# Kernel optimization log

Hardware: AMD Instinct MI355X
Metric: run time of the kernel (lower is better)

The kernel has to match this reference:

```python
import jax, jax.numpy as jnp
import numpy as np


def _mlp(h, weights, biases, n_relu):
    # Linear(+ReLU) stack; ReLU on the first n_relu layers, final layer linear only.
    for i, (w, b) in enumerate(zip(weights, biases)):
        h = h @ w + b
        if i < n_relu:
            h = jax.nn.relu(h)
    return h


def setup_inputs() -> dict:
    key = jax.random.key(0)
    ks = jax.random.split(key, 12)
    B, M, E = 16384, 512, 1024

    def lin(k, fan_in, fan_out):
        # xavier-ish scaling so activations stay well-conditioned
        return jax.random.normal(k, (fan_in, fan_out), jnp.float32) * (1.0 / np.sqrt(fan_in))

    return {
        "x": jax.random.normal(ks[0], (B, M), jnp.float32),
        "rand_noise": jax.random.uniform(ks[1], (B, M), jnp.float32),
        "u_random": jax.random.uniform(ks[2], (B, M), jnp.float32),
        "marginals_min": jnp.zeros((M,), jnp.float32),
        "marginals_max": jnp.ones((M,), jnp.float32),
        "enc_w0": lin(ks[3], M, E), "enc_b0": jnp.full((E,), 0.01, jnp.float32),
        "enc_w1": lin(ks[4], E, E), "enc_b1": jnp.full((E,), 0.01, jnp.float32),
        "enc_w2": lin(ks[5], E, E), "enc_b2": jnp.full((E,), 0.01, jnp.float32),
        "enc_w3": lin(ks[6], E, E), "enc_b3": jnp.full((E,), 0.01, jnp.float32),
        "head_w0": lin(ks[7], E, E), "head_b0": jnp.full((E,), 0.01, jnp.float32),
        "head_w1": lin(ks[8], E, E), "head_b1": jnp.full((E,), 0.01, jnp.float32),
        "corruption_len": 307,
    }


def reference(x, rand_noise, u_random, marginals_min, marginals_max,
              enc_w0, enc_b0, enc_w1, enc_b1, enc_w2, enc_b2, enc_w3, enc_b3,
              head_w0, head_b0, head_w1, head_b1, corruption_len):
    B, M = x.shape
    # Vectorized equivalent of per-row randperm(m)[:corruption_len]:
    # top-k of iid uniform noise picks a uniform random subset of size k per row.
    _, idx = jax.lax.top_k(rand_noise, corruption_len)            # [B, k]
    mask = jnp.zeros((B, M), bool).at[jnp.arange(B)[:, None], idx].set(True)

    # Marginal samples ~ Uniform(min, max) per feature.
    x_random = marginals_min + u_random * (marginals_max - marginals_min)
    x_corrupted = jnp.where(mask, x_random, x)

    enc_ws = [enc_w0, enc_w1, enc_w2, enc_w3]
    enc_bs = [enc_b0, enc_b1, enc_b2, enc_b3]
    head_ws = [head_w0, head_w1]
    head_bs = [head_b0, head_b1]

    # Run both branches through one batched pass (same math, fewer launches).
    both = jnp.concatenate([x, x_corrupted], axis=0)              # [2B, M]
    h = _mlp(both, enc_ws, enc_bs, n_relu=3)                      # encoder depth 4
    h = _mlp(h, head_ws, head_bs, n_relu=1)                       # head depth 2
    embeddings, embeddings_corrupted = h[:B], h[B:]
    return embeddings, embeddings_corrupted
```

## Files before the change

### kernel.cpp

```cpp
#include <hip/hip_runtime.h>

typedef _Float16 f16x8 __attribute__((ext_vector_type(8)));
typedef float f32x4 __attribute__((ext_vector_type(4)));

__device__ __forceinline__ void gload16(const void* g, void* l) {
  __builtin_amdgcn_global_load_lds(
      (const __attribute__((address_space(1))) void*)g,
      (__attribute__((address_space(3))) void*)l, 16, 0, 0);
}

__device__ __forceinline__ void barfence() {
  asm volatile("" ::: "memory");
  __builtin_amdgcn_s_barrier();
  asm volatile("" ::: "memory");
}

__device__ __forceinline__ int xcd_swz(int orig, int nwg) {
  int q = nwg >> 3, r = nwg & 7;
  int x = orig & 7, loc = orig >> 3;
  int base = (x < r) ? x * (q + 1) : r * (q + 1) + (x - r) * q;
  return base + loc;
}

struct WPtrs { const float* w[6]; _Float16* wt[6]; };
__global__ __launch_bounds__(256) void transpose_all(WPtrs p) {
  const int N = 1024;
  __shared__ float tile[32][33];
  int y = blockIdx.y, layer, ky;
  if (y < 16) { layer = 0; ky = y; }
  else { int t = y - 16; layer = 1 + (t >> 5); ky = t & 31; }
  int K = (layer == 0) ? 512 : 1024;
  const float* W = p.w[layer];
  _Float16* WT = p.wt[layer];
  int tx = threadIdx.x, ty = threadIdx.y;
  int n0 = blockIdx.x * 32, k0 = ky * 32;
#pragma unroll
  for (int i = 0; i < 4; i++)
    tile[ty + i * 8][tx] = W[(long)(k0 + ty + i * 8) * N + (n0 + tx)];
  __syncthreads();
#pragma unroll
  for (int i = 0; i < 4; i++)
    WT[(long)(n0 + ty + i * 8) * K + (k0 + tx)] = (_Float16)tile[tx][ty + i * 8];
}

__global__ __launch_bounds__(256) void cast_f16(const float* __restrict__ in,
                                                _Float16* __restrict__ out, long n) {
  long i = ((long)blockIdx.x * 256 + threadIdx.x) * 4;
  if (i < n) {
    float4 v = *(const float4*)(in + i);
    typedef _Float16 f16x4 __attribute__((ext_vector_type(4)));
    f16x4 o = {(_Float16)v.x, (_Float16)v.y, (_Float16)v.z, (_Float16)v.w};
    *(f16x4*)(out + i) = o;
  }
}

__global__ __launch_bounds__(256) void topk_corrupt(
    const float* __restrict__ noise, const float* __restrict__ x,
    const float* __restrict__ u, const float* __restrict__ mmin,
    const float* __restrict__ mmax, const int* __restrict__ kptr,
    _Float16* __restrict__ dplain, _Float16* __restrict__ dcorr,
    int xrow0, int nrows) {
  int lane = threadIdx.x & 63;
  int r = (blockIdx.x << 2) + (threadIdx.x >> 6);
  if (r >= nrows) return;
  long row = (long)xrow0 + r;
  long rb = row * 512 + lane * 8;
  float4 n0 = *(const float4*)(noise + rb);
  float4 n1 = *(const float4*)(noise + rb + 4);
  unsigned v[8] = {__float_as_uint(n0.x), __float_as_uint(n0.y),
                   __float_as_uint(n0.z), __float_as_uint(n0.w),
                   __float_as_uint(n1.x), __float_as_uint(n1.y),
                   __float_as_uint(n1.z), __float_as_uint(n1.w)};
  int kk = *kptr;
  unsigned T = 0;
  for (int bit = 30; bit >= 0; --bit) {
    unsigned Tp = T | (1u << bit);
    int c = 0;
#pragma unroll
    for (int j = 0; j < 8; j++) c += (int)__popcll(__ballot(v[j] >= Tp));
    if (c >= kk) T = Tp;
  }
  int cgt = 0;
  unsigned long long eqb[8];
#pragma unroll
  for (int j = 0; j < 8; j++) {
    cgt += (int)__popcll(__ballot(v[j] > T));
    eqb[j] = __ballot(v[j] == T);
  }
  int need = kk - cgt;
  unsigned long long below = (1ull << lane) - 1ull;
  int rank_base = 0;
#pragma unroll
  for (int j = 0; j < 8; j++) rank_base += (int)__popcll(eqb[j] & below);

  float4 x0 = *(const float4*)(x + rb);
  float4 x1 = *(const float4*)(x + rb + 4);
  float4 u0 = *(const float4*)(u + rb);
  float4 u1 = *(const float4*)(u + rb + 4);
  int col = lane * 8;
  float4 mn0 = *(const float4*)(mmin + col);
  float4 mn1 = *(const float4*)(mmin + col + 4);
  float4 mx0 = *(const float4*)(mmax + col);
  float4 mx1 = *(const float4*)(mmax + col + 4);
  float xs[8] = {x0.x, x0.y, x0.z, x0.w, x1.x, x1.y, x1.z, x1.w};
  float us[8] = {u0.x, u0.y, u0.z, u0.w, u1.x, u1.y, u1.z, u1.w};
  float mns[8] = {mn0.x, mn0.y, mn0.z, mn0.w, mn1.x, mn1.y, mn1.z, mn1.w};
  float mxs[8] = {mx0.x, mx0.y, mx0.z, mx0.w, mx1.x, mx1.y, mx1.z, mx1.w};

  f16x8 po, co;
  int loc = 0;
#pragma unroll
  for (int j = 0; j < 8; j++) {
    bool eq = (v[j] == T);
    int rank = rank_base + loc;
    bool m = (v[j] > T) || (eq && (rank < need));
    loc += eq ? 1 : 0;
    float rv = mns[j] + us[j] * (mxs[j] - mns[j]);
    float cv = m ? rv : xs[j];
    po[j] = (_Float16)xs[j];
    co[j] = (_Float16)cv;
  }
  long ob = (long)r * 512 + lane * 8;
  if (dplain) *(f16x8*)(dplain + ob) = po;
  *(f16x8*)(dcorr + ob) = co;
}

template <bool RELU, bool OUTF32>
__global__ __launch_bounds__(512, 2) void gemm8p(const _Float16* __restrict__ A,
                                                 const _Float16* __restrict__ BT,
                                                 const float* __restrict__ bias,
                                                 void* __restrict__ Cout, int K) {
  const int N = 1024;
  __shared__ _Float16 S[2][4][8192];
  int tid = threadIdx.x;
  int lane = tid & 63, wave = tid >> 6;
  int wr = wave >> 2, wc = wave & 3;
  int logical = xcd_swz(blockIdx.x, gridDim.x);
  long arow0 = (long)(logical >> 2) * 256;
  int bcol0 = (logical & 3) * 256;

  int srow = tid >> 3;
  int scg = (tid & 7) ^ (srow & 7);
  const _Float16* gA[2][2];
  const _Float16* gB[2][2];
#pragma unroll
  for (int h = 0; h < 2; h++)
#pragma unroll
    for (int j = 0; j < 2; j++) {
      gA[h][j] = A + (arow0 + h * 128 + j * 64 + srow) * (long)K + scg * 8;
      gB[h][j] = BT + (long)(bcol0 + h * 128 + j * 64 + srow) * K + scg * 8;
    }
  int lo = tid * 8;

#define STG_A(BUF, H, T)                                   \
  do {                                                     \
    gload16(gA[H][0] + (T) * 64, &S[BUF][H][lo]);          \
    gload16(gA[H][1] + (T) * 64, &S[BUF][H][4096 + lo]);   \
  } while (0)
#define STG_B(BUF, H, T)                                      \
  do {                                                        \
    gload16(gB[H][0] + (T) * 64, &S[BUF][2 + H][lo]);         \
    gload16(gB[H][1] + (T) * 64, &S[BUF][2 + H][4096 + lo]);  \
  } while (0)

  int lr = lane & 15, g = lane >> 4, e = lr & 7;
  int cs0 = ((0 * 4 + g) ^ e) * 8;
  int cs1 = ((1 * 4 + g) ^ e) * 8;
  int aoff[4], boff[2];
#pragma unroll
  for (int mf = 0; mf < 4; mf++) aoff[mf] = (wr * 64 + mf * 16 + lr) * 64;
#pragma unroll
  for (int nf = 0; nf < 2; nf++) boff[nf] = (wc * 32 + nf * 16 + lr) * 64;

  f16x8 af0[4][2], af1[4][2];
  f16x8 bf[2][2][2];
  f32x4 acc[2][2][4][2] = {};

#define LDA(DST, BUF, MQ)                                            \
  do {                                                               \
    _Pragma("unroll") for (int mf = 0; mf < 4; mf++) {               \
      DST[mf][0] = *(const f16x8*)&S[BUF][MQ][aoff[mf] + cs0];       \
      DST[mf][1] = *(const f16x8*)&S[BUF][MQ][aoff[mf] + cs1];       \
    }                                                                \
  } while (0)
#define LDB(BUF, NQ)                                                 \
  do {                                                               \
    _Pragma("unroll") for (int nf = 0; nf < 2; nf++) {               \
      bf[NQ][nf][0] = *(const f16x8*)&S[BUF][2 + NQ][boff[nf] + cs0];\
      bf[NQ][nf][1] = *(const f16x8*)&S[BUF][2 + NQ][boff[nf] + cs1];\
    }                                                                \
  } while (0)
#define MFMA_Q(AF, MQ, NQ)                                           \
  do {                                                               \
    __builtin_amdgcn_s_setprio(1);                                   \
    _Pragma("unroll") for (int mf = 0; mf < 4; mf++)                 \
    _Pragma("unroll") for (int nf = 0; nf < 2; nf++)                 \
    _Pragma("unroll") for (int kk = 0; kk < 2; kk++)                 \
      acc[MQ][NQ][mf][nf] = __builtin_amdgcn_mfma_f32_16x16x32_f16(  \
          AF[mf][kk], bf[NQ][nf][kk], acc[MQ][NQ][mf][nf], 0, 0, 0); \
    __builtin_amdgcn_s_setprio(0);                                   \
  } while (0)

  int NT = K / 64;
  STG_A(0, 0, 0); STG_B(0, 0, 0); STG_A(0, 1, 0); STG_B(0, 1, 0);
  if (NT > 1) {
    STG_A(1, 0, 1); STG_B(1, 0, 1);
    asm volatile("s_waitcnt vmcnt(4)" ::: "memory");
  } else {
    asm volatile("s_waitcnt vmcnt(0)" ::: "memory");
  }
  barfence();

  for (int t = 0; t < NT; ++t) {
    int buf = t & 1, nbuf = buf ^ 1;
    LDB(buf, 0);
    LDA(af0, buf, 0);
    LDB(buf, 1);
    if (t + 1 < NT) { STG_A(nbuf, 1, t + 1); STG_B(nbuf, 1, t + 1); }
    MFMA_Q(af0, 0, 0);
    barfence();
    LDA(af1, buf, 1);
    if (t + 2 < NT) STG_A(buf, 0, t + 2);
    MFMA_Q(af0, 0, 1);
    barfence();
    if (t + 2 < NT) STG_B(buf, 0, t + 2);
    MFMA_Q(af1, 1, 0);
    barfence();
    if (t + 1 < NT) {
      if (t + 2 < NT) asm volatile("s_waitcnt vmcnt(4)" ::: "memory");
      else            asm volatile("s_waitcnt vmcnt(0)" ::: "memory");
    }
    MFMA_Q(af1, 1, 1);
    if (t + 1 < NT) barfence();
  }
#undef STG_A
#undef STG_B
#undef LDA
#undef LDB
#undef MFMA_Q

  int r0 = (lane >> 4) * 4;
  float bv[2][2];
#pragma unroll
  for (int nq = 0; nq < 2; nq++)
#pragma unroll
    for (int nf = 0; nf < 2; nf++)
      bv[nq][nf] = bias[bcol0 + nq * 128 + wc * 32 + nf * 16 + lr];
#pragma unroll
  for (int mq = 0; mq < 2; mq++)
#pragma unroll
    for (int mf = 0; mf < 4; mf++) {
      long rowb = arow0 + mq * 128 + wr * 64 + mf * 16 + r0;
#pragma unroll
      for (int nq = 0; nq < 2; nq++)
#pragma unroll
        for (int nf = 0; nf < 2; nf++) {
          int col = bcol0 + nq * 128 + wc * 32 + nf * 16 + lr;
#pragma unroll
          for (int rr = 0; rr < 4; rr++) {
            float v = acc[mq][nq][mf][nf][rr] + bv[nq][nf];
            if (RELU) v = fmaxf(v, 0.f);
            if (OUTF32) ((float*)Cout)[(rowb + rr) * N + col] = v;
            else ((_Float16*)Cout)[(rowb + rr) * N + col] = (_Float16)v;
          }
        }
    }
}

extern "C" void kernel_launch(void* const* d_in, const int* in_sizes, int n_in,
                              void* d_out, int out_size, void* d_ws, size_t ws_size,
                              hipStream_t stream) {
  const float* x    = (const float*)d_in[0];
  const float* rn   = (const float*)d_in[1];
  const float* ur   = (const float*)d_in[2];
  const float* mmin = (const float*)d_in[3];
  const float* mmax = (const float*)d_in[4];
  const float* W[6]  = {(const float*)d_in[5],  (const float*)d_in[7],  (const float*)d_in[9],
                        (const float*)d_in[11], (const float*)d_in[13], (const float*)d_in[15]};
  const float* Bi[6] = {(const float*)d_in[6],  (const float*)d_in[8],  (const float*)d_in[10],
                        (const float*)d_in[12], (const float*)d_in[14], (const float*)d_in[16]};
  const int* kptr = (const int*)d_in[17];
  float* out = (float*)d_out;

  const long B = 16384;
  const int E = 1024;
  const int Ks[6] = {512, 1024, 1024, 1024, 1024, 1024};

  char* ws = (char*)d_ws;
  _Float16* wT[6];
  size_t off = 0;
  for (int i = 0; i < 6; i++) { wT[i] = (_Float16*)(ws + off); off += (size_t)Ks[i] * E * 2; }
  size_t rem = (ws_size > off) ? ws_size - off : 0;
  long R = 32768;
  while (R > 256 && (size_t)R * 5120 > rem) R >>= 1;

  _Float16* bothc = (_Float16*)(ws + off);
  _Float16* h0 = bothc + R * 512;
  _Float16* h1 = h0 + R * 1024;

  WPtrs wp;
  for (int i = 0; i < 6; i++) { wp.w[i] = W[i]; wp.wt[i] = wT[i]; }
  transpose_all<<<dim3(E / 32, 16 + 5 * 32), dim3(32, 8), 0, stream>>>(wp);

  for (long r0 = 0; r0 < 2 * B; r0 += R) {
    if (R == 2 * B) {
      topk_corrupt<<<dim3((unsigned)(B / 4)), dim3(256), 0, stream>>>(
          rn, x, ur, mmin, mmax, kptr, bothc, bothc + B * 512, 0, (int)B);
    } else {
      long plainEnd = (r0 < B) ? ((r0 + R < B) ? (r0 + R) : B) : r0;
      long p1 = plainEnd - r0;
      if (p1 > 0) {
        long n = p1 * 512;
        long blocks = (n / 4 + 255) / 256;
        cast_f16<<<dim3((unsigned)blocks), dim3(256), 0, stream>>>(x + r0 * 512, bothc, n);
      }
      long c0 = (r0 > B) ? r0 : B;
      long p2 = (r0 + R) - c0;
      if (p2 > 0) {
        topk_corrupt<<<dim3((unsigned)((p2 + 3) / 4)), dim3(256), 0, stream>>>(
            rn, x, ur, mmin, mmax, kptr, (_Float16*)nullptr,
            bothc + (c0 - r0) * 512, (int)(c0 - B), (int)p2);
      }
    }
    dim3 gg((unsigned)((R / 256) * 4)), gb(512);
    gemm8p<true,  false><<<gg, gb, 0, stream>>>(bothc, wT[0], Bi[0], (void*)h0, 512);
    gemm8p<true,  false><<<gg, gb, 0, stream>>>(h0,    wT[1], Bi[1], (void*)h1, 1024);
    gemm8p<true,  false><<<gg, gb, 0, stream>>>(h1,    wT[2], Bi[2], (void*)h0, 1024);
    gemm8p<false, false><<<gg, gb, 0, stream>>>(h0,    wT[3], Bi[3], (void*)h1, 1024);
    gemm8p<true,  false><<<gg, gb, 0, stream>>>(h1,    wT[4], Bi[4], (void*)h0, 1024);
    gemm8p<false, true ><<<gg, gb, 0, stream>>>(h0,    wT[5], Bi[5],
                                                 (void*)(out + r0 * 1024), 1024);
  }
}
```

Measured before the change: 404.6 us.

## Restructure GEMM main loop staging order and register double-buffer B fragments

```diff
diff --git a/kernel.cpp b/kernel.cpp
--- a/kernel.cpp
+++ b/kernel.cpp
@@ -173,7 +173,7 @@
   for (int nf = 0; nf < 2; nf++) boff[nf] = (wc * 32 + nf * 16 + lr) * 64;
 
   f16x8 af0[4][2], af1[4][2];
-  f16x8 bf[2][2][2];
+  f16x8 bf0[2][2], bf1[2][2];
   f32x4 acc[2][2][4][2] = {};
 
 #define LDA(DST, BUF, MQ)                                            \
@@ -183,54 +183,49 @@
       DST[mf][1] = *(const f16x8*)&S[BUF][MQ][aoff[mf] + cs1];       \
     }                                                                \
   } while (0)
-#define LDB(BUF, NQ)                                                 \
+#define LDB(DST, BUF, NQ)                                            \
   do {                                                               \
     _Pragma("unroll") for (int nf = 0; nf < 2; nf++) {               \
-      bf[NQ][nf][0] = *(const f16x8*)&S[BUF][2 + NQ][boff[nf] + cs0];\
-      bf[NQ][nf][1] = *(const f16x8*)&S[BUF][2 + NQ][boff[nf] + cs1];\
+      DST[nf][0] = *(const f16x8*)&S[BUF][2 + NQ][boff[nf] + cs0];   \
+      DST[nf][1] = *(const f16x8*)&S[BUF][2 + NQ][boff[nf] + cs1];   \
     }                                                                \
   } while (0)
-#define MFMA_Q(AF, MQ, NQ)                                           \
+#define MFMA_Q(AF, BF, MQ, NQ)                                       \
   do {                                                               \
     __builtin_amdgcn_s_setprio(1);                                   \
     _Pragma("unroll") for (int mf = 0; mf < 4; mf++)                 \
     _Pragma("unroll") for (int nf = 0; nf < 2; nf++)                 \
     _Pragma("unroll") for (int kk = 0; kk < 2; kk++)                 \
       acc[MQ][NQ][mf][nf] = __builtin_amdgcn_mfma_f32_16x16x32_f16(  \
-          AF[mf][kk], bf[NQ][nf][kk], acc[MQ][NQ][mf][nf], 0, 0, 0); \
+          AF[mf][kk], BF[nf][kk], acc[MQ][NQ][mf][nf], 0, 0, 0);     \
     __builtin_amdgcn_s_setprio(0);                                   \
   } while (0)
 
   int NT = K / 64;
-  STG_A(0, 0, 0); STG_B(0, 0, 0); STG_A(0, 1, 0); STG_B(0, 1, 0);
-  if (NT > 1) {
-    STG_A(1, 0, 1); STG_B(1, 0, 1);
-    asm volatile("s_waitcnt vmcnt(4)" ::: "memory");
-  } else {
-    asm volatile("s_waitcnt vmcnt(0)" ::: "memory");
-  }
+  STG_B(0, 0, 0); STG_B(0, 1, 0); STG_A(0, 0, 0); STG_A(0, 1, 0);
+  asm volatile("s_waitcnt vmcnt(2)" ::: "memory");
   barfence();
+  LDA(af0, 0, 0);
+  LDB(bf1, 0, 1);
 
   for (int t = 0; t < NT; ++t) {
     int buf = t & 1, nbuf = buf ^ 1;
-    LDB(buf, 0);
-    LDA(af0, buf, 0);
-    LDB(buf, 1);
-    if (t + 1 < NT) { STG_A(nbuf, 1, t + 1); STG_B(nbuf, 1, t + 1); }
-    MFMA_Q(af0, 0, 0);
+    LDB(bf0, buf, 0);
+    if (t + 1 < NT) { STG_B(nbuf, 0, t + 1); STG_B(nbuf, 1, t + 1); }
+    MFMA_Q(af0, bf0, 0, 0);
+    if (t + 1 < NT) asm volatile("s_waitcnt vmcnt(4)" ::: "memory");
+    else            asm volatile("s_waitcnt vmcnt(0)" ::: "memory");
     barfence();
     LDA(af1, buf, 1);
-    if (t + 2 < NT) STG_A(buf, 0, t + 2);
-    MFMA_Q(af0, 0, 1);
+    if (t + 1 < NT) STG_A(nbuf, 0, t + 1);
+    MFMA_Q(af0, bf1, 0, 1);
     barfence();
-    if (t + 2 < NT) STG_B(buf, 0, t + 2);
-    MFMA_Q(af1, 1, 0);
+    if (t + 1 < NT) STG_A(nbuf, 1, t + 1);
+    MFMA_Q(af1, bf1, 1, 1);
+    if (t + 1 < NT) asm volatile("s_waitcnt vmcnt(2)" ::: "memory");
     barfence();
-    if (t + 1 < NT) {
-      if (t + 2 < NT) asm volatile("s_waitcnt vmcnt(4)" ::: "memory");
-      else            asm volatile("s_waitcnt vmcnt(0)" ::: "memory");
-    }
-    MFMA_Q(af1, 1, 1);
+    if (t + 1 < NT) { LDA(af0, nbuf, 0); LDB(bf1, nbuf, 1); }
+    MFMA_Q(af1, bf0, 1, 0);
     if (t + 1 < NT) barfence();
   }
 #undef STG_A
```

Measured after the change: 404.7 us. No clear change (+0.0%).

## Replace 256x256 quadrant-pipelined GEMM with 128x128 tile, simple double buffer

Applied to the files above, without the earlier changes.

```diff
diff --git a/kernel.cpp b/kernel.cpp
--- a/kernel.cpp
+++ b/kernel.cpp
@@ -126,41 +126,36 @@
 }
 
 template <bool RELU, bool OUTF32>
-__global__ __launch_bounds__(512, 2) void gemm8p(const _Float16* __restrict__ A,
+__global__ __launch_bounds__(512, 4) void gemm2b(const _Float16* __restrict__ A,
                                                  const _Float16* __restrict__ BT,
                                                  const float* __restrict__ bias,
                                                  void* __restrict__ Cout, int K) {
   const int N = 1024;
-  __shared__ _Float16 S[2][4][8192];
+  __shared__ _Float16 S[2][2][8192];
   int tid = threadIdx.x;
   int lane = tid & 63, wave = tid >> 6;
   int wr = wave >> 2, wc = wave & 3;
   int logical = xcd_swz(blockIdx.x, gridDim.x);
-  long arow0 = (long)(logical >> 2) * 256;
-  int bcol0 = (logical & 3) * 256;
+  long arow0 = (long)(logical >> 3) * 128;
+  int bcol0 = (logical & 7) * 128;
 
   int srow = tid >> 3;
   int scg = (tid & 7) ^ (srow & 7);
-  const _Float16* gA[2][2];
-  const _Float16* gB[2][2];
-#pragma unroll
-  for (int h = 0; h < 2; h++)
-#pragma unroll
-    for (int j = 0; j < 2; j++) {
-      gA[h][j] = A + (arow0 + h * 128 + j * 64 + srow) * (long)K + scg * 8;
-      gB[h][j] = BT + (long)(bcol0 + h * 128 + j * 64 + srow) * K + scg * 8;
-    }
+  const _Float16* gA[2];
+  const _Float16* gB[2];
+#pragma unroll
+  for (int j = 0; j < 2; j++) {
+    gA[j] = A + (arow0 + j * 64 + srow) * (long)K + scg * 8;
+    gB[j] = BT + (long)(bcol0 + j * 64 + srow) * K + scg * 8;
+  }
   int lo = tid * 8;
 
-#define STG_A(BUF, H, T)                                   \
-  do {                                                     \
-    gload16(gA[H][0] + (T) * 64, &S[BUF][H][lo]);          \
-    gload16(gA[H][1] + (T) * 64, &S[BUF][H][4096 + lo]);   \
-  } while (0)
-#define STG_B(BUF, H, T)                                      \
-  do {                                                        \
-    gload16(gB[H][0] + (T) * 64, &S[BUF][2 + H][lo]);         \
-    gload16(gB[H][1] + (T) * 64, &S[BUF][2 + H][4096 + lo]);  \
+#define STG(BUF, T)                                     \
+  do {                                                  \
+    gload16(gA[0] + (T) * 64, &S[BUF][0][lo]);          \
+    gload16(gA[1] + (T) * 64, &S[BUF][0][4096 + lo]);   \
+    gload16(gB[0] + (T) * 64, &S[BUF][1][lo]);          \
+    gload16(gB[1] + (T) * 64, &S[BUF][1][4096 + lo]);   \
   } while (0)
 
   int lr = lane & 15, g = lane >> 4, e = lr & 7;
@@ -172,99 +167,66 @@
 #pragma unroll
   for (int nf = 0; nf < 2; nf++) boff[nf] = (wc * 32 + nf * 16 + lr) * 64;
 
-  f16x8 af0[4][2], af1[4][2];
-  f16x8 bf[2][2][2];
-  f32x4 acc[2][2][4][2] = {};
-
-#define LDA(DST, BUF, MQ)                                            \
-  do {                                                               \
-    _Pragma("unroll") for (int mf = 0; mf < 4; mf++) {               \
-      DST[mf][0] = *(const f16x8*)&S[BUF][MQ][aoff[mf] + cs0];       \
-      DST[mf][1] = *(const f16x8*)&S[BUF][MQ][aoff[mf] + cs1];       \
-    }                                                                \
-  } while (0)
-#define LDB(BUF, NQ)                                                 \
-  do {                                                               \
-    _Pragma("unroll") for (int nf = 0; nf < 2; nf++) {               \
-      bf[NQ][nf][0] = *(const f16x8*)&S[BUF][2 + NQ][boff[nf] + cs0];\
-      bf[NQ][nf][1] = *(const f16x8*)&S[BUF][2 + NQ][boff[nf] + cs1];\
-    }                                                                \
-  } while (0)
-#define MFMA_Q(AF, MQ, NQ)                                           \
-  do {                                                               \
-    __builtin_amdgcn_s_setprio(1);                                   \
-    _Pragma("unroll") for (int mf = 0; mf < 4; mf++)                 \
-    _Pragma("unroll") for (int nf = 0; nf < 2; nf++)                 \
-    _Pragma("unroll") for (int kk = 0; kk < 2; kk++)                 \
-      acc[MQ][NQ][mf][nf] = __builtin_amdgcn_mfma_f32_16x16x32_f16(  \
-          AF[mf][kk], bf[NQ][nf][kk], acc[MQ][NQ][mf][nf], 0, 0, 0); \
-    __builtin_amdgcn_s_setprio(0);                                   \
-  } while (0)
+  f16x8 af[4][2], bf[2][2];
+  f32x4 acc[4][2] = {};
 
   int NT = K / 64;
-  STG_A(0, 0, 0); STG_B(0, 0, 0); STG_A(0, 1, 0); STG_B(0, 1, 0);
-  if (NT > 1) {
-    STG_A(1, 0, 1); STG_B(1, 0, 1);
-    asm volatile("s_waitcnt vmcnt(4)" ::: "memory");
-  } else {
-    asm volatile("s_waitcnt vmcnt(0)" ::: "memory");
-  }
+  STG(0, 0);
+  asm volatile("s_waitcnt vmcnt(0)" ::: "memory");
   barfence();
 
   for (int t = 0; t < NT; ++t) {
     int buf = t & 1, nbuf = buf ^ 1;
-    LDB(buf, 0);
-    LDA(af0, buf, 0);
-    LDB(buf, 1);
-    if (t + 1 < NT) { STG_A(nbuf, 1, t + 1); STG_B(nbuf, 1, t + 1); }
-    MFMA_Q(af0, 0, 0);
-    barfence();
-    LDA(af1, buf, 1);
-    if (t + 2 < NT) STG_A(buf, 0, t + 2);
-    MFMA_Q(af0, 0, 1);
-    barfence();
-    if (t + 2 < NT) STG_B(buf, 0, t + 2);
-    MFMA_Q(af1, 1, 0);
-    barfence();
+    if (t + 1 < NT) STG(nbuf, t + 1);
+#pragma unroll
+    for (int mf = 0; mf < 4; mf++) {
+      af[mf][0] = *(const f16x8*)&S[buf][0][aoff[mf] + cs0];
+      af[mf][1] = *(const f16x8*)&S[buf][0][aoff[mf] + cs1];
+    }
+#pragma unroll
+    for (int nf = 0; nf < 2; nf++) {
+      bf[nf][0] = *(const f16x8*)&S[buf][1][boff[nf] + cs0];
+      bf[nf][1] = *(const f16x8*)&S[buf][1][boff[nf] + cs1];
+    }
+    __builtin_amdgcn_s_setprio(1);
+#pragma unroll
+    for (int mf = 0; mf < 4; mf++)
+#pragma unroll
+      for (int nf = 0; nf < 2; nf++)
+#pragma unroll
+        for (int kk = 0; kk < 2; kk++)
+          acc[mf][nf] = __builtin_amdgcn_mfma_f32_16x16x32_f16(
+              af[mf][kk], bf[nf][kk], acc[mf][nf], 0, 0, 0);
+    __builtin_amdgcn_s_setprio(0);
     if (t + 1 < NT) {
-      if (t + 2 < NT) asm volatile("s_waitcnt vmcnt(4)" ::: "memory");
-      else            asm volatile("s_waitcnt vmcnt(0)" ::: "memory");
-    }
-    MFMA_Q(af1, 1, 1);
-    if (t + 1 < NT) barfence();
-  }
-#undef STG_A
-#undef STG_B
-#undef LDA
-#undef LDB
-#undef MFMA_Q
+      asm volatile("s_waitcnt vmcnt(0)" ::: "memory");
+      barfence();
+    }
+  }
+#undef STG
 
   int r0 = (lane >> 4) * 4;
-  float bv[2][2];
-#pragma unroll
-  for (int nq = 0; nq < 2; nq++)
-#pragma unroll
-    for (int nf = 0; nf < 2; nf++)
-      bv[nq][nf] = bias[bcol0 + nq * 128 + wc * 32 + nf * 16 + lr];
-#pragma unroll
-  for (int mq = 0; mq < 2; mq++)
-#pragma unroll
-    for (int mf = 0; mf < 4; mf++) {
-      long rowb = arow0 + mq * 128 + wr * 64 + mf * 16 + r0;
-#pragma unroll
-      for (int nq = 0; nq < 2; nq++)
-#pragma unroll
-        for (int nf = 0; nf < 2; nf++) {
-          int col = bcol0 + nq * 128 + wc * 32 + nf * 16 + lr;
-#pragma unroll
-          for (int rr = 0; rr < 4; rr++) {
-            float v = acc[mq][nq][mf][nf][rr] + bv[nq][nf];
-            if (RELU) v = fmaxf(v, 0.f);
-            if (OUTF32) ((float*)Cout)[(rowb + rr) * N + col] = v;
-            else ((_Float16*)Cout)[(rowb + rr) * N + col] = (_Float16)v;
-          }
+  float bv[2];
+#pragma unroll
+  for (int nf = 0; nf < 2; nf++) bv[nf] = bias[bcol0 + wc * 32 + nf * 16 + lr];
+#pragma unroll
+  for (int mf = 0; mf < 4; mf++) {
+    long rowb = arow0 + wr * 64 + mf * 16 + r0;
+#pragma unroll
+    for (int nf = 0; nf < 2; nf++) {
+      int col = bcol0 + wc * 32 + nf * 16 + lr;
+#pragma unroll
+      for (int rr = 0; rr < 4; rr++) {
+        float v = acc[mf][nf][rr] + bv[nf];
+        if (RELU) v = fmaxf(v, 0.f);
+        if (OUTF32) {
+          __builtin_nontemporal_store(v, &((float*)Cout)[(rowb + rr) * N + col]);
+        } else {
+          ((_Float16*)Cout)[(rowb + rr) * N + col] = (_Float16)v;
         }
-    }
+      }
+    }
+  }
 }
 
 extern "C" void kernel_launch(void* const* d_in, const int* in_sizes, int n_in,
@@ -292,7 +254,7 @@
   for (int i = 0; i < 6; i++) { wT[i] = (_Float16*)(ws + off); off += (size_t)Ks[i] * E * 2; }
   size_t rem = (ws_size > off) ? ws_size - off : 0;
   long R = 32768;
-  while (R > 256 && (size_t)R * 5120 > rem) R >>= 1;
+  while (R > 128 && (size_t)R * 5120 > rem) R >>= 1;
 
   _Float16* bothc = (_Float16*)(ws + off);
   _Float16* h0 = bothc + R * 512;
@@ -322,13 +284,13 @@
             bothc + (c0 - r0) * 512, (int)(c0 - B), (int)p2);
       }
     }
-    dim3 gg((unsigned)((R / 256) * 4)), gb(512);
-    gemm8p<true,  false><<<gg, gb, 0, stream>>>(bothc, wT[0], Bi[0], (void*)h0, 512);
-    gemm8p<true,  false><<<gg, gb, 0, stream>>>(h0,    wT[1], Bi[1], (void*)h1, 1024);
-    gemm8p<true,  false><<<gg, gb, 0, stream>>>(h1,    wT[2], Bi[2], (void*)h0, 1024);
-    gemm8p<false, false><<<gg, gb, 0, stream>>>(h0,    wT[3], Bi[3], (void*)h1, 1024);
-    gemm8p<true,  false><<<gg, gb, 0, stream>>>(h1,    wT[4], Bi[4], (void*)h0, 1024);
-    gemm8p<false, true ><<<gg, gb, 0, stream>>>(h0,    wT[5], Bi[5],
+    dim3 gg((unsigned)((R / 128) * 8)), gb(512);
+    gemm2b<true,  false><<<gg, gb, 0, stream>>>(bothc, wT[0], Bi[0], (void*)h0, 512);
+    gemm2b<true,  false><<<gg, gb, 0, stream>>>(h0,    wT[1], Bi[1], (void*)h1, 1024);
+    gemm2b<true,  false><<<gg, gb, 0, stream>>>(h1,    wT[2], Bi[2], (void*)h0, 1024);
+    gemm2b<false, false><<<gg, gb, 0, stream>>>(h0,    wT[3], Bi[3], (void*)h1, 1024);
+    gemm2b<true,  false><<<gg, gb, 0, stream>>>(h1,    wT[4], Bi[4], (void*)h0, 1024);
+    gemm2b<false, true ><<<gg, gb, 0, stream>>>(h0,    wT[5], Bi[5],
                                                  (void*)(out + r0 * 1024), 1024);
   }
 }
```

Result: slower. 420.1 us (+3.8%).
